# Kernel tuning notes

Measured on AMD Instinct MI355X. Metric: run time of the kernel, lower is better.

Reference implementation:

```python
import jax, jax.numpy as jnp
import numpy as np

DIM = 1024
N_HEADS = 16
HEAD_DIM = DIM // N_HEADS
LN_EPS = 1e-5


def layer_norm(x, gamma, beta):
    mu = jnp.mean(x, axis=-1, keepdims=True)
    var = jnp.var(x, axis=-1, keepdims=True)
    return (x - mu) * jax.lax.rsqrt(var + LN_EPS) * gamma + beta


def setup_inputs() -> dict:
    key = jax.random.key(0)
    ks = jax.random.split(key, 12)
    B, Nq, Nc, D = 2, 2048, 2048, DIM
    s = 1.0 / np.sqrt(D)
    return {
        "query": jax.random.normal(ks[0], (B, Nq, D), jnp.float32),
        "context": jax.random.normal(ks[1], (B, Nc, D), jnp.float32),
        "Wq": jax.random.normal(ks[2], (D, D), jnp.float32) * s,
        "bq": jnp.zeros((D,), jnp.float32),
        "Wk": jax.random.normal(ks[3], (D, D), jnp.float32) * s,
        "bk": jnp.zeros((D,), jnp.float32),
        "Wv": jax.random.normal(ks[4], (D, D), jnp.float32) * s,
        "bv": jnp.zeros((D,), jnp.float32),
        "Wo": jax.random.normal(ks[5], (D, D), jnp.float32) * s,
        "bo": jnp.zeros((D,), jnp.float32),
        "gq": jnp.ones((D,), jnp.float32),
        "betaq": jnp.zeros((D,), jnp.float32),
        "gkv": jnp.ones((D,), jnp.float32),
        "betakv": jnp.zeros((D,), jnp.float32),
    }


def reference(query, context, Wq, bq, Wk, bk, Wv, bv, Wo, bo, gq, betaq, gkv, betakv):
    B, Nq, D = query.shape
    Nc = context.shape[1]
    residual = query
    q = layer_norm(query, gq, betaq)
    c = layer_norm(context, gkv, betakv)
    # projections; (B,N,D) -> (B,H,N,hd)
    Q = (q @ Wq + bq).reshape(B, Nq, N_HEADS, HEAD_DIM).transpose(0, 2, 1, 3)
    K = (c @ Wk + bk).reshape(B, Nc, N_HEADS, HEAD_DIM).transpose(0, 2, 1, 3)
    V = (c @ Wv + bv).reshape(B, Nc, N_HEADS, HEAD_DIM).transpose(0, 2, 1, 3)
    scores = jnp.einsum("bhqd,bhkd->bhqk", Q, K) / np.sqrt(HEAD_DIM).astype(np.float32)
    attn = jax.nn.softmax(scores, axis=-1)
    out = jnp.einsum("bhqk,bhkd->bhqd", attn, V)
    out = out.transpose(0, 2, 1, 3).reshape(B, Nq, D)
    return residual + out @ Wo + bo
```

## Files before the change

kernel.cpp:

```cpp
#include <hip/hip_runtime.h>
#include <hip/hip_bf16.h>

typedef unsigned short u16;
typedef unsigned long long u64;
typedef __bf16 bf16x8 __attribute__((ext_vector_type(8)));
typedef float f32x4 __attribute__((ext_vector_type(4)));

#define DIM 1024
#define NH 16
#define HD 64
#define QSCALE 0.180336880972788f

__device__ __forceinline__ u16 f2bf(float f) {
  union { float f; unsigned u; } v; v.f = f;
  unsigned r = v.u + 0x7fffu + ((v.u >> 16) & 1u);
  return (u16)(r >> 16);
}

__device__ __forceinline__ unsigned pk2(float a, float b) {
  union { __hip_bfloat162 h; unsigned u; } cv;
  cv.h = __float22bfloat162_rn(make_float2(a, b));
  return cv.u;
}

__device__ __forceinline__ float bf2f(unsigned s) {
  union { unsigned u; float f; } v; v.u = s << 16; return v.f;
}

__device__ __forceinline__ float fexp2(float x) {
#if __has_builtin(__builtin_amdgcn_exp2f)
  return __builtin_amdgcn_exp2f(x);
#else
  return exp2f(x);
#endif
}

__device__ __forceinline__ void gld16(const u16* gp, u16* lp) {
  __builtin_amdgcn_global_load_lds(
      (const __attribute__((address_space(1))) unsigned int*)(const void*)gp,
      (__attribute__((address_space(3))) unsigned int*)(void*)lp, 16, 0, 0);
}

__global__ __launch_bounds__(256) void prep_kernel(
    const float* __restrict__ q, const float* __restrict__ c,
    const float* __restrict__ gq, const float* __restrict__ bq,
    const float* __restrict__ gkv, const float* __restrict__ bkv,
    u16* __restrict__ qn, u16* __restrict__ cn,
    const float* W0, const float* W1, const float* W2, const float* W3,
    u16* O0, u16* O1, u16* O2, u16* O3) {
  __shared__ float red[2][4];
  __shared__ float t[32][33];
  int bid = blockIdx.x, tid = threadIdx.x;
  if (bid < 8192) {
    const float* x  = bid < 4096 ? q : c;
    const float* g  = bid < 4096 ? gq : gkv;
    const float* be = bid < 4096 ? bq : bkv;
    u16* out = bid < 4096 ? qn : cn;
    int row = bid & 4095;
    float4 v = ((const float4*)(x + (size_t)row * DIM))[tid];
    float s1 = v.x + v.y + v.z + v.w;
    float s2 = v.x * v.x + v.y * v.y + v.z * v.z + v.w * v.w;
#pragma unroll
    for (int o = 32; o >= 1; o >>= 1) { s1 += __shfl_xor(s1, o, 64); s2 += __shfl_xor(s2, o, 64); }
    int wv = tid >> 6;
    if ((tid & 63) == 0) { red[0][wv] = s1; red[1][wv] = s2; }
    __syncthreads();
    s1 = red[0][0] + red[0][1] + red[0][2] + red[0][3];
    s2 = red[1][0] + red[1][1] + red[1][2] + red[1][3];
    float mu = s1 * (1.f / DIM);
    float var = s2 * (1.f / DIM) - mu * mu;
    float rs = rsqrtf(var + 1e-5f);
    float4 gv = ((const float4*)g)[tid];
    float4 bv = ((const float4*)be)[tid];
    uint2 o2;
    o2.x = pk2((v.x - mu) * rs * gv.x + bv.x, (v.y - mu) * rs * gv.y + bv.y);
    o2.y = pk2((v.z - mu) * rs * gv.z + bv.z, (v.w - mu) * rs * gv.w + bv.w);
    ((uint2*)(out + (size_t)row * DIM))[tid] = o2;
  } else {
    int wid = bid - 8192;
    int z = wid >> 10;
    const float* W = z == 0 ? W0 : z == 1 ? W1 : z == 2 ? W2 : W3;
    u16* O        = z == 0 ? O0 : z == 1 ? O1 : z == 2 ? O2 : O3;
    int xy = wid & 1023;
    int bx = (xy & 31) * 32, by = (xy >> 5) * 32;
    int tx = tid & 31, ty = tid >> 5;
#pragma unroll
    for (int i = 0; i < 4; ++i) t[ty + i * 8][tx] = W[(size_t)(by + ty + i * 8) * DIM + bx + tx];
    __syncthreads();
#pragma unroll
    for (int i = 0; i < 4; ++i) O[(size_t)(bx + ty + i * 8) * DIM + by + tx] = f2bf(t[tx][ty + i * 8]);
  }
}

struct GArg { const u16* A; const u16* Bt; const float* bias; void* out; int mode; };
struct GArg3 { GArg g[3]; };

__global__ __launch_bounds__(256) void gemm128(GArg3 args) {
  GArg ga = args.g[blockIdx.z];
  const u16* __restrict__ A  = ga.A;
  const u16* __restrict__ Bt = ga.Bt;
  __shared__ __align__(16) u16 sm[128 * 64 * 2];
  u16* As = sm;
  u16* Bs = sm + 128 * 64;
  int tid = threadIdx.x, wave = tid >> 6, lane = tid & 63;
  int lr = lane & 15, quad = lane >> 4;
  int m0 = blockIdx.x * 128, n0 = blockIdx.y * 128;
  int wm = (wave >> 1) * 64, wn = (wave & 1) * 64;
  int mode = ga.mode;
  f32x4 acc[4][4] = {};
  for (int kt = 0; kt < DIM; kt += 64) {
#pragma unroll
    for (int r = 0; r < 4; ++r) {
      int slot = tid + r * 256;
      int row = slot >> 3;
      int c = (slot & 7) ^ (row & 7);
      gld16(A + (size_t)(m0 + row) * DIM + kt + c * 8, &As[slot * 8]);
    }
#pragma unroll
    for (int r = 0; r < 4; ++r) {
      int slot = tid + r * 256;
      int row = slot >> 3;
      int c = (slot & 7) ^ (row & 7);
      gld16(Bt + (size_t)(n0 + row) * DIM + kt + c * 8, &Bs[slot * 8]);
    }
    __syncthreads();
#pragma unroll
    for (int kc = 0; kc < 2; ++kc) {
      int pc = ((kc * 4 + quad) ^ (lr & 7)) * 8;
      bf16x8 af[4], bfr[4];
#pragma unroll
      for (int i = 0; i < 4; ++i) {
        af[i]  = *(const bf16x8*)&As[(wm + i * 16 + lr) * 64 + pc];
        bfr[i] = *(const bf16x8*)&Bs[(wn + i * 16 + lr) * 64 + pc];
      }
      if (mode != 2) {
#pragma unroll
        for (int mi = 0; mi < 4; ++mi)
#pragma unroll
          for (int ni = 0; ni < 4; ++ni)
            acc[mi][ni] = __builtin_amdgcn_mfma_f32_16x16x32_bf16(af[mi], bfr[ni], acc[mi][ni], 0, 0, 0);
      } else {
#pragma unroll
        for (int mi = 0; mi < 4; ++mi)
#pragma unroll
          for (int ni = 0; ni < 4; ++ni)
            acc[mi][ni] = __builtin_amdgcn_mfma_f32_16x16x32_bf16(bfr[ni], af[mi], acc[mi][ni], 0, 0, 0);
      }
    }
    __syncthreads();
  }
  const float* bias = ga.bias;
  if (mode == 2) {
#pragma unroll
    for (int mi = 0; mi < 4; ++mi) {
      int m = m0 + wm + mi * 16 + lr;
      int bb = m >> 11, tt = m & 2047;
      u16* outb = (u16*)ga.out + (((size_t)bb << 10)) * 2048 + tt;
#pragma unroll
      for (int ni = 0; ni < 4; ++ni) {
        int nbase = n0 + wn + ni * 16 + quad * 4;
#pragma unroll
        for (int r = 0; r < 4; ++r)
          outb[(size_t)(nbase + r) * 2048] = f2bf(acc[mi][ni][r] + bias[nbase + r]);
      }
    }
  } else {
    float sc = (mode == 1) ? QSCALE : 1.f;
#pragma unroll
    for (int mi = 0; mi < 4; ++mi)
#pragma unroll
      for (int ni = 0; ni < 4; ++ni) {
        int col = n0 + wn + ni * 16 + lr;
        float bv = bias[col];
        int row0 = m0 + wm + mi * 16 + quad * 4;
#pragma unroll
        for (int r = 0; r < 4; ++r)
          ((u16*)ga.out)[(size_t)(row0 + r) * DIM + col] = f2bf((acc[mi][ni][r] + bv) * sc);
      }
  }
}

__global__ __launch_bounds__(256) void gemm_o(const u16* __restrict__ A,
    const u16* __restrict__ Bt, const float* __restrict__ bias,
    float* __restrict__ out, const float* __restrict__ resid) {
  __shared__ __align__(16) u16 sm[(128 + 64) * 64];
  u16* As = sm;
  u16* Bs = sm + 128 * 64;
  int tid = threadIdx.x, wave = tid >> 6, lane = tid & 63;
  int lr = lane & 15, quad = lane >> 4;
  int m0 = blockIdx.x * 128, n0 = blockIdx.y * 64;
  int wm = (wave >> 1) * 64, wn = (wave & 1) * 32;
  f32x4 acc[4][2] = {};
  for (int kt = 0; kt < DIM; kt += 64) {
#pragma unroll
    for (int r = 0; r < 4; ++r) {
      int slot = tid + r * 256;
      int row = slot >> 3;
      int c = (slot & 7) ^ (row & 7);
      gld16(A + (size_t)(m0 + row) * DIM + kt + c * 8, &As[slot * 8]);
    }
#pragma unroll
    for (int r = 0; r < 2; ++r) {
      int slot = tid + r * 256;
      int row = slot >> 3;
      int c = (slot & 7) ^ (row & 7);
      gld16(Bt + (size_t)(n0 + row) * DIM + kt + c * 8, &Bs[slot * 8]);
    }
    __syncthreads();
#pragma unroll
    for (int kc = 0; kc < 2; ++kc) {
      int pc = ((kc * 4 + quad) ^ (lr & 7)) * 8;
      bf16x8 af[4], bfr[2];
#pragma unroll
      for (int i = 0; i < 4; ++i) af[i] = *(const bf16x8*)&As[(wm + i * 16 + lr) * 64 + pc];
#pragma unroll
      for (int j = 0; j < 2; ++j) bfr[j] = *(const bf16x8*)&Bs[(wn + j * 16 + lr) * 64 + pc];
#pragma unroll
      for (int mi = 0; mi < 4; ++mi)
#pragma unroll
        for (int ni = 0; ni < 2; ++ni)
          acc[mi][ni] = __builtin_amdgcn_mfma_f32_16x16x32_bf16(af[mi], bfr[ni], acc[mi][ni], 0, 0, 0);
    }
    __syncthreads();
  }
#pragma unroll
  for (int mi = 0; mi < 4; ++mi)
#pragma unroll
    for (int ni = 0; ni < 2; ++ni) {
      int col = n0 + wn + ni * 16 + lr;
      float bv = bias[col];
      int row0 = m0 + wm + mi * 16 + quad * 4;
#pragma unroll
      for (int r = 0; r < 4; ++r) {
        int row = row0 + r;
        out[(size_t)row * DIM + col] = acc[mi][ni][r] + bv + resid[(size_t)row * DIM + col];
      }
    }
}

__global__ __launch_bounds__(256) void flash_kernel(const u16* __restrict__ Q,
    const u16* __restrict__ Kg, const u16* __restrict__ Vt,
    u16* __restrict__ O0, u16* __restrict__ O1,
    float* __restrict__ L0, float* __restrict__ L1) {
  __shared__ __align__(16) u16 lds[20480];
  int tid = threadIdx.x, wave = tid >> 6, lane = tid & 63;
  int lr = lane & 15, quad = lane >> 4;
  int bh = blockIdx.x, b = bh >> 4, h = bh & 15;
  int q0 = blockIdx.y * 128;
  int split = blockIdx.z;
  u16* Op = split ? O1 : O0;
  float* Lp = split ? L1 : L0;
  int t0 = split * 1024;

  const u16* kbase = Kg + (size_t)(b * 2048 + t0) * DIM + h * HD;
  const u16* vbase = Vt + (size_t)(b * 1024 + h * HD) * 2048 + t0;

  bf16x8 qf[2][2];
#pragma unroll
  for (int s = 0; s < 2; ++s)
#pragma unroll
    for (int kc = 0; kc < 2; ++kc)
      qf[s][kc] = *(const bf16x8*)&Q[((size_t)(b * 2048 + q0 + wave * 32 + s * 16 + lr)) * DIM +
                                     h * HD + kc * 32 + quad * 8];

  int slot0 = tid, slot1 = tid + 256;
  int r0 = slot0 >> 3, c0 = (slot0 & 7) ^ (r0 & 7);
  int r1 = slot1 >> 3, c1 = (slot1 & 7) ^ (r1 & 7);
  const u16* kp0 = kbase + (size_t)r0 * DIM + c0 * 8;
  const u16* kp1 = kbase + (size_t)r1 * DIM + c1 * 8;
  const u16* vp0 = vbase + (size_t)r0 * 2048 + c0 * 8;
  const u16* vp1 = vbase + (size_t)r1 * 2048 + c1 * 8;

  gld16(kp0, &lds[slot0 * 8]);
  gld16(kp1, &lds[slot1 * 8]);
  gld16(vp0, &lds[8192 + slot0 * 8]);
  gld16(vp1, &lds[8192 + slot1 * 8]);
  __syncthreads();

  u16* Pw = &lds[16384 + wave * 1024];
  float plsum[2] = {0.f, 0.f};
  f32x4 oacc[2][4] = {};

  for (int j = 0; j < 16; ++j) {
    int par = j & 1;
    const u16* kcb = &lds[par * 4096];
    const u16* vcb = &lds[8192 + par * 4096];
    if (j < 15) {
      int np = par ^ 1;
      kp0 += 64 * DIM; kp1 += 64 * DIM; vp0 += 64; vp1 += 64;
      gld16(kp0, &lds[np * 4096 + slot0 * 8]);
      gld16(kp1, &lds[np * 4096 + slot1 * 8]);
      gld16(vp0, &lds[8192 + np * 4096 + slot0 * 8]);
      gld16(vp1, &lds[8192 + np * 4096 + slot1 * 8]);
    }

    f32x4 sf[2][4] = {};
#pragma unroll
    for (int kc = 0; kc < 2; ++kc) {
      int pc = ((kc * 4 + quad) ^ (lr & 7)) * 8;
#pragma unroll
      for (int ns = 0; ns < 4; ++ns) {
        bf16x8 kf = *(const bf16x8*)&kcb[(ns * 16 + lr) * 64 + pc];
#pragma unroll
        for (int s = 0; s < 2; ++s)
          sf[s][ns] = __builtin_amdgcn_mfma_f32_16x16x32_bf16(kf, qf[s][kc], sf[s][ns], 0, 0, 0);
      }
    }

#pragma unroll
    for (int kc = 0; kc < 2; ++kc) {
#pragma unroll
      for (int s = 0; s < 2; ++s)
#pragma unroll
        for (int nsl = 0; nsl < 2; ++nsl) {
          int ns = kc * 2 + nsl;
          float p0 = fexp2(sf[s][ns][0]), p1 = fexp2(sf[s][ns][1]);
          float p2 = fexp2(sf[s][ns][2]), p3 = fexp2(sf[s][ns][3]);
          plsum[s] += (p0 + p1) + (p2 + p3);
          uint2 pk;
          pk.x = pk2(p0, p1);
          pk.y = pk2(p2, p3);
          int pp = (((nsl * 2 + (quad >> 1)) ^ (lr & 3)) * 8) + (quad & 1) * 4;
          *(uint2*)&Pw[(s * 16 + lr) * 32 + pp] = pk;
        }
      __threadfence_block();
      int pvc = ((kc * 4 + quad) ^ (lr & 7)) * 8;
      bf16x8 pf[2];
#pragma unroll
      for (int s = 0; s < 2; ++s)
        pf[s] = *(const bf16x8*)&Pw[(s * 16 + lr) * 32 + ((quad ^ (lr & 3)) * 8)];
#pragma unroll
      for (int ds = 0; ds < 4; ++ds) {
        bf16x8 vf = *(const bf16x8*)&vcb[(ds * 16 + lr) * 64 + pvc];
#pragma unroll
        for (int s = 0; s < 2; ++s)
          oacc[s][ds] = __builtin_amdgcn_mfma_f32_16x16x32_bf16(vf, pf[s], oacc[s][ds], 0, 0, 0);
      }
    }
    __syncthreads();
  }

#pragma unroll
  for (int s = 0; s < 2; ++s) {
    float l = plsum[s];
    l += __shfl_xor(l, 16, 64);
    l += __shfl_xor(l, 32, 64);
    size_t qrow = (size_t)(b * 2048 + q0 + wave * 32 + s * 16 + lr);
    if (quad == 0) Lp[qrow * 16 + h] = l;
#pragma unroll
    for (int ds = 0; ds < 4; ++ds) {
      uint2 pk;
      pk.x = pk2(oacc[s][ds][0], oacc[s][ds][1]);
      pk.y = pk2(oacc[s][ds][2], oacc[s][ds][3]);
      *(uint2*)&Op[qrow * DIM + h * HD + ds * 16 + quad * 4] = pk;
    }
  }
}

__global__ __launch_bounds__(256) void combine_kernel(const u16* __restrict__ O0,
    const u16* __restrict__ O1, const float* __restrict__ L0, const float* __restrict__ L1,
    u16* __restrict__ AO) {
  int row = blockIdx.x, tid = threadIdx.x;
  int h = tid >> 4;
  float rl = 1.f / (L0[row * 16 + h] + L1[row * 16 + h]);
  uint2 a = ((const uint2*)(O0 + (size_t)row * DIM))[tid];
  uint2 b = ((const uint2*)(O1 + (size_t)row * DIM))[tid];
  float v0 = (bf2f(a.x & 0xffff) + bf2f(b.x & 0xffff)) * rl;
  float v1 = (bf2f(a.x >> 16)    + bf2f(b.x >> 16))    * rl;
  float v2 = (bf2f(a.y & 0xffff) + bf2f(b.y & 0xffff)) * rl;
  float v3 = (bf2f(a.y >> 16)    + bf2f(b.y >> 16))    * rl;
  uint2 o;
  o.x = pk2(v0, v1);
  o.y = pk2(v2, v3);
  ((uint2*)(AO + (size_t)row * DIM))[tid] = o;
}

extern "C" void kernel_launch(void* const* d_in, const int* in_sizes, int n_in,
                              void* d_out, int out_size, void* d_ws, size_t ws_size,
                              hipStream_t stream) {
  const float* query   = (const float*)d_in[0];
  const float* context = (const float*)d_in[1];
  const float* Wq = (const float*)d_in[2];
  const float* bq = (const float*)d_in[3];
  const float* Wk = (const float*)d_in[4];
  const float* bk = (const float*)d_in[5];
  const float* Wv = (const float*)d_in[6];
  const float* bv = (const float*)d_in[7];
  const float* Wo = (const float*)d_in[8];
  const float* bo = (const float*)d_in[9];
  const float* gq    = (const float*)d_in[10];
  const float* betaq = (const float*)d_in[11];
  const float* gkv   = (const float*)d_in[12];
  const float* betakv= (const float*)d_in[13];
  (void)in_sizes; (void)n_in; (void)out_size; (void)ws_size;

  char* ws = (char*)d_ws;
  const size_t MB = (size_t)1 << 20;
  u16* qn  = (u16*)(ws + 0 * MB);
  u16* cn  = (u16*)(ws + 8 * MB);
  u16* Wqt = (u16*)(ws + 16 * MB);
  u16* Wkt = (u16*)(ws + 18 * MB);
  u16* Wvt = (u16*)(ws + 20 * MB);
  u16* Wot = (u16*)(ws + 22 * MB);
  u16* Qb  = (u16*)(ws + 24 * MB);
  u16* Kb  = (u16*)(ws + 32 * MB);
  u16* Vtb = (u16*)(ws + 40 * MB);
  u16* AOb = (u16*)(ws + 48 * MB);
  u16* Op0 = qn;
  u16* Op1 = cn;
  float* L0 = (float*)(ws + 16 * MB);
  float* L1 = (float*)(ws + 16 * MB + 256 * 1024);

  prep_kernel<<<12288, 256, 0, stream>>>(query, context, gq, betaq, gkv, betakv,
                                         qn, cn, Wq, Wk, Wv, Wo, Wqt, Wkt, Wvt, Wot);

  GArg3 a3;
  a3.g[0] = { qn, Wqt, bq, (void*)Qb,  1 };
  a3.g[1] = { cn, Wkt, bk, (void*)Kb,  0 };
  a3.g[2] = { cn, Wvt, bv, (void*)Vtb, 2 };
  gemm128<<<dim3(32, 8, 3), 256, 0, stream>>>(a3);

  flash_kernel<<<dim3(32, 16, 2), 256, 0, stream>>>(Qb, Kb, Vtb, Op0, Op1, L0, L1);

  combine_kernel<<<4096, 256, 0, stream>>>(Op0, Op1, L0, L1, AOb);

  gemm_o<<<dim3(32, 16), 256, 0, stream>>>(AOb, Wot, bo, (float*)d_out, query);
}
```

Before: 246.8 us.

## Fuse K/V projections sharing context tile and batch P writes in flash kernel

```diff
diff --git a/kernel.cpp b/kernel.cpp
--- a/kernel.cpp
+++ b/kernel.cpp
@@ -92,90 +92,130 @@
   }
 }
 
-struct GArg { const u16* A; const u16* Bt; const float* bias; void* out; int mode; };
-struct GArg3 { GArg g[3]; };
-
-__global__ __launch_bounds__(256) void gemm128(GArg3 args) {
-  GArg ga = args.g[blockIdx.z];
-  const u16* __restrict__ A  = ga.A;
-  const u16* __restrict__ Bt = ga.Bt;
-  __shared__ __align__(16) u16 sm[128 * 64 * 2];
-  u16* As = sm;
-  u16* Bs = sm + 128 * 64;
+__global__ __launch_bounds__(256) void gemm_qkv(
+    const u16* __restrict__ qn, const u16* __restrict__ cn,
+    const u16* __restrict__ Wqt, const u16* __restrict__ Wkt, const u16* __restrict__ Wvt,
+    const float* __restrict__ bq, const float* __restrict__ bk, const float* __restrict__ bv,
+    u16* __restrict__ Qb, u16* __restrict__ Kb, u16* __restrict__ Vtb) {
+  __shared__ __align__(16) u16 sm[(128 + 64 + 64) * 64];
+  u16* As  = sm;
+  u16* B0s = sm + 128 * 64;
+  u16* B1s = sm + 192 * 64;
   int tid = threadIdx.x, wave = tid >> 6, lane = tid & 63;
   int lr = lane & 15, quad = lane >> 4;
-  int m0 = blockIdx.x * 128, n0 = blockIdx.y * 128;
-  int wm = (wave >> 1) * 64, wn = (wave & 1) * 64;
-  int mode = ga.mode;
-  f32x4 acc[4][4] = {};
-  for (int kt = 0; kt < DIM; kt += 64) {
-#pragma unroll
-    for (int r = 0; r < 4; ++r) {
-      int slot = tid + r * 256;
-      int row = slot >> 3;
-      int c = (slot & 7) ^ (row & 7);
-      gld16(A + (size_t)(m0 + row) * DIM + kt + c * 8, &As[slot * 8]);
-    }
-#pragma unroll
-    for (int r = 0; r < 4; ++r) {
-      int slot = tid + r * 256;
-      int row = slot >> 3;
-      int c = (slot & 7) ^ (row & 7);
-      gld16(Bt + (size_t)(n0 + row) * DIM + kt + c * 8, &Bs[slot * 8]);
-    }
-    __syncthreads();
-#pragma unroll
-    for (int kc = 0; kc < 2; ++kc) {
-      int pc = ((kc * 4 + quad) ^ (lr & 7)) * 8;
-      bf16x8 af[4], bfr[4];
-#pragma unroll
-      for (int i = 0; i < 4; ++i) {
-        af[i]  = *(const bf16x8*)&As[(wm + i * 16 + lr) * 64 + pc];
-        bfr[i] = *(const bf16x8*)&Bs[(wn + i * 16 + lr) * 64 + pc];
-      }
-      if (mode != 2) {
+  int m0 = blockIdx.x * 128, n0 = blockIdx.y * 64;
+  int wm = (wave >> 1) * 64, wn = (wave & 1) * 32;
+
+  if (blockIdx.z == 0) {
+    f32x4 acck[4][2] = {}, accv[4][2] = {};
+    for (int kt = 0; kt < DIM; kt += 64) {
+#pragma unroll
+      for (int r = 0; r < 4; ++r) {
+        int slot = tid + r * 256;
+        int row = slot >> 3;
+        int c = (slot & 7) ^ (row & 7);
+        gld16(cn + (size_t)(m0 + row) * DIM + kt + c * 8, &As[slot * 8]);
+      }
+      {
+        int slot = tid;
+        int row = slot >> 3;
+        int c = (slot & 7) ^ (row & 7);
+        gld16(Wkt + (size_t)(n0 + row) * DIM + kt + c * 8, &B0s[slot * 8]);
+        gld16(Wvt + (size_t)(n0 + row) * DIM + kt + c * 8, &B1s[slot * 8]);
+        slot = tid + 256; row = slot >> 3; c = (slot & 7) ^ (row & 7);
+        gld16(Wkt + (size_t)(n0 + row) * DIM + kt + c * 8, &B0s[slot * 8]);
+        gld16(Wvt + (size_t)(n0 + row) * DIM + kt + c * 8, &B1s[slot * 8]);
+      }
+      __syncthreads();
+#pragma unroll
+      for (int kc = 0; kc < 2; ++kc) {
+        int pc = ((kc * 4 + quad) ^ (lr & 7)) * 8;
+        bf16x8 af[4], b0f[2], b1f[2];
+#pragma unroll
+        for (int i = 0; i < 4; ++i) af[i] = *(const bf16x8*)&As[(wm + i * 16 + lr) * 64 + pc];
+#pragma unroll
+        for (int j = 0; j < 2; ++j) {
+          b0f[j] = *(const bf16x8*)&B0s[(wn + j * 16 + lr) * 64 + pc];
+          b1f[j] = *(const bf16x8*)&B1s[(wn + j * 16 + lr) * 64 + pc];
+        }
 #pragma unroll
         for (int mi = 0; mi < 4; ++mi)
 #pragma unroll
-          for (int ni = 0; ni < 4; ++ni)
-            acc[mi][ni] = __builtin_amdgcn_mfma_f32_16x16x32_bf16(af[mi], bfr[ni], acc[mi][ni], 0, 0, 0);
-      } else {
-#pragma unroll
-        for (int mi = 0; mi < 4; ++mi)
-#pragma unroll
-          for (int ni = 0; ni < 4; ++ni)
-            acc[mi][ni] = __builtin_amdgcn_mfma_f32_16x16x32_bf16(bfr[ni], af[mi], acc[mi][ni], 0, 0, 0);
-      }
-    }
-    __syncthreads();
-  }
-  const float* bias = ga.bias;
-  if (mode == 2) {
+          for (int ni = 0; ni < 2; ++ni) {
+            acck[mi][ni] = __builtin_amdgcn_mfma_f32_16x16x32_bf16(af[mi], b0f[ni], acck[mi][ni], 0, 0, 0);
+            accv[mi][ni] = __builtin_amdgcn_mfma_f32_16x16x32_bf16(b1f[ni], af[mi], accv[mi][ni], 0, 0, 0);
+          }
+      }
+      __syncthreads();
+    }
+#pragma unroll
+    for (int mi = 0; mi < 4; ++mi)
+#pragma unroll
+      for (int ni = 0; ni < 2; ++ni) {
+        int col = n0 + wn + ni * 16 + lr;
+        float bb_ = bk[col];
+        int row0 = m0 + wm + mi * 16 + quad * 4;
+#pragma unroll
+        for (int r = 0; r < 4; ++r)
+          Kb[(size_t)(row0 + r) * DIM + col] = f2bf(acck[mi][ni][r] + bb_);
+      }
 #pragma unroll
     for (int mi = 0; mi < 4; ++mi) {
       int m = m0 + wm + mi * 16 + lr;
       int bb = m >> 11, tt = m & 2047;
-      u16* outb = (u16*)ga.out + (((size_t)bb << 10)) * 2048 + tt;
-#pragma unroll
-      for (int ni = 0; ni < 4; ++ni) {
+      u16* outb = Vtb + (((size_t)bb << 10)) * 2048 + tt;
+#pragma unroll
+      for (int ni = 0; ni < 2; ++ni) {
         int nbase = n0 + wn + ni * 16 + quad * 4;
 #pragma unroll
         for (int r = 0; r < 4; ++r)
-          outb[(size_t)(nbase + r) * 2048] = f2bf(acc[mi][ni][r] + bias[nbase + r]);
+          outb[(size_t)(nbase + r) * 2048] = f2bf(accv[mi][ni][r] + bv[nbase + r]);
       }
     }
   } else {
-    float sc = (mode == 1) ? QSCALE : 1.f;
+    f32x4 acc[4][2] = {};
+    for (int kt = 0; kt < DIM; kt += 64) {
+#pragma unroll
+      for (int r = 0; r < 4; ++r) {
+        int slot = tid + r * 256;
+        int row = slot >> 3;
+        int c = (slot & 7) ^ (row & 7);
+        gld16(qn + (size_t)(m0 + row) * DIM + kt + c * 8, &As[slot * 8]);
+      }
+#pragma unroll
+      for (int r = 0; r < 2; ++r) {
+        int slot = tid + r * 256;
+        int row = slot >> 3;
+        int c = (slot & 7) ^ (row & 7);
+        gld16(Wqt + (size_t)(n0 + row) * DIM + kt + c * 8, &B0s[slot * 8]);
+      }
+      __syncthreads();
+#pragma unroll
+      for (int kc = 0; kc < 2; ++kc) {
+        int pc = ((kc * 4 + quad) ^ (lr & 7)) * 8;
+        bf16x8 af[4], b0f[2];
+#pragma unroll
+        for (int i = 0; i < 4; ++i) af[i] = *(const bf16x8*)&As[(wm + i * 16 + lr) * 64 + pc];
+#pragma unroll
+        for (int j = 0; j < 2; ++j) b0f[j] = *(const bf16x8*)&B0s[(wn + j * 16 + lr) * 64 + pc];
+#pragma unroll
+        for (int mi = 0; mi < 4; ++mi)
+#pragma unroll
+          for (int ni = 0; ni < 2; ++ni)
+            acc[mi][ni] = __builtin_amdgcn_mfma_f32_16x16x32_bf16(af[mi], b0f[ni], acc[mi][ni], 0, 0, 0);
+      }
+      __syncthreads();
+    }
 #pragma unroll
     for (int mi = 0; mi < 4; ++mi)
 #pragma unroll
-      for (int ni = 0; ni < 4; ++ni) {
+      for (int ni = 0; ni < 2; ++ni) {
         int col = n0 + wn + ni * 16 + lr;
-        float bv = bias[col];
+        float bb_ = bq[col];
         int row0 = m0 + wm + mi * 16 + quad * 4;
 #pragma unroll
         for (int r = 0; r < 4; ++r)
-          ((u16*)ga.out)[(size_t)(row0 + r) * DIM + col] = f2bf((acc[mi][ni][r] + bv) * sc);
+          Qb[(size_t)(row0 + r) * DIM + col] = f2bf((acc[mi][ni][r] + bb_) * QSCALE);
       }
   }
 }
@@ -242,7 +282,7 @@
     const u16* __restrict__ Kg, const u16* __restrict__ Vt,
     u16* __restrict__ O0, u16* __restrict__ O1,
     float* __restrict__ L0, float* __restrict__ L1) {
-  __shared__ __align__(16) u16 lds[20480];
+  __shared__ __align__(16) u16 lds[24576];
   int tid = threadIdx.x, wave = tid >> 6, lane = tid & 63;
   int lr = lane & 15, quad = lane >> 4;
   int bh = blockIdx.x, b = bh >> 4, h = bh & 15;
@@ -277,7 +317,7 @@
   gld16(vp1, &lds[8192 + slot1 * 8]);
   __syncthreads();
 
-  u16* Pw = &lds[16384 + wave * 1024];
+  u16* Pw = &lds[16384 + wave * 2048];
   float plsum[2] = {0.f, 0.f};
   f32x4 oacc[2][4] = {};
 
@@ -308,30 +348,31 @@
     }
 
 #pragma unroll
+    for (int s = 0; s < 2; ++s)
+#pragma unroll
+      for (int ns = 0; ns < 4; ++ns) {
+        float p0 = fexp2(sf[s][ns][0]), p1 = fexp2(sf[s][ns][1]);
+        float p2 = fexp2(sf[s][ns][2]), p3 = fexp2(sf[s][ns][3]);
+        plsum[s] += (p0 + p1) + (p2 + p3);
+        uint2 pk;
+        pk.x = pk2(p0, p1);
+        pk.y = pk2(p2, p3);
+        int chunk = ns * 2 + (quad >> 1);
+        int off = (s * 16 + lr) * 64 + ((chunk ^ (lr & 7)) * 8) + (quad & 1) * 4;
+        *(uint2*)&Pw[off] = pk;
+      }
+    __threadfence_block();
+
+#pragma unroll
     for (int kc = 0; kc < 2; ++kc) {
+      int pc = ((kc * 4 + quad) ^ (lr & 7)) * 8;
+      bf16x8 pf[2];
 #pragma unroll
       for (int s = 0; s < 2; ++s)
-#pragma unroll
-        for (int nsl = 0; nsl < 2; ++nsl) {
-          int ns = kc * 2 + nsl;
-          float p0 = fexp2(sf[s][ns][0]), p1 = fexp2(sf[s][ns][1]);
-          float p2 = fexp2(sf[s][ns][2]), p3 = fexp2(sf[s][ns][3]);
-          plsum[s] += (p0 + p1) + (p2 + p3);
-          uint2 pk;
-          pk.x = pk2(p0, p1);
-          pk.y = pk2(p2, p3);
-          int pp = (((nsl * 2 + (quad >> 1)) ^ (lr & 3)) * 8) + (quad & 1) * 4;
-          *(uint2*)&Pw[(s * 16 + lr) * 32 + pp] = pk;
-        }
-      __threadfence_block();
-      int pvc = ((kc * 4 + quad) ^ (lr & 7)) * 8;
-      bf16x8 pf[2];
-#pragma unroll
-      for (int s = 0; s < 2; ++s)
-        pf[s] = *(const bf16x8*)&Pw[(s * 16 + lr) * 32 + ((quad ^ (lr & 3)) * 8)];
+        pf[s] = *(const bf16x8*)&Pw[(s * 16 + lr) * 64 + pc];
 #pragma unroll
       for (int ds = 0; ds < 4; ++ds) {
-        bf16x8 vf = *(const bf16x8*)&vcb[(ds * 16 + lr) * 64 + pvc];
+        bf16x8 vf = *(const bf16x8*)&vcb[(ds * 16 + lr) * 64 + pc];
 #pragma unroll
         for (int s = 0; s < 2; ++s)
           oacc[s][ds] = __builtin_amdgcn_mfma_f32_16x16x32_bf16(vf, pf[s], oacc[s][ds], 0, 0, 0);
@@ -414,11 +455,8 @@
   prep_kernel<<<12288, 256, 0, stream>>>(query, context, gq, betaq, gkv, betakv,
                                          qn, cn, Wq, Wk, Wv, Wo, Wqt, Wkt, Wvt, Wot);
 
-  GArg3 a3;
-  a3.g[0] = { qn, Wqt, bq, (void*)Qb,  1 };
-  a3.g[1] = { cn, Wkt, bk, (void*)Kb,  0 };
-  a3.g[2] = { cn, Wvt, bv, (void*)Vtb, 2 };
-  gemm128<<<dim3(32, 8, 3), 256, 0, stream>>>(a3);
+  gemm_qkv<<<dim3(32, 16, 2), 256, 0, stream>>>(qn, cn, Wqt, Wkt, Wvt,
+                                                bq, bk, bv, Qb, Kb, Vtb);
 
   flash_kernel<<<dim3(32, 16, 2), 256, 0, stream>>>(Qb, Kb, Vtb, Op0, Op1, L0, L1);
 
```

After: 220.9 us. 10.5% less time.
